# Kernel optimization log

Hardware: AMD Instinct MI355X
Metric: run time of the kernel (lower is better)

The kernel has to match this reference:

```python
import jax, jax.numpy as jnp
import numpy as np

EPS = 1e-12

def _pdist(a, b):
    # a: [B,N,3], b: [B,M,3] -> [B,N,M] L2 distances (no huge [B,N,M,3] temp)
    sq = (jnp.sum(a * a, -1)[:, :, None] + jnp.sum(b * b, -1)[:, None, :]
          - 2.0 * jnp.einsum('bnd,bmd->bnm', a, b))
    return jnp.sqrt(jnp.maximum(sq, EPS))

def _loss_terms(skel_xyz, skel_radius, skel_nori, l3_xyz, shape_all):
    normal = shape_all[:, :, 3:6]
    shape_xyz = shape_all[:, :, :3]
    B, Ns, _ = skel_xyz.shape
    N = shape_xyz.shape[1]

    # --- loss_sample: 8 surface samples per sphere ---
    e = 0.57735027
    dirs = jnp.array([[e, e, e], [e, e, -e], [e, -e, e], [e, -e, -e],
                      [-e, e, e], [-e, e, -e], [-e, -e, e], [-e, -e, -e]],
                     dtype=skel_xyz.dtype)
    centers = jnp.repeat(skel_xyz, 8, axis=1)
    radii = jnp.repeat(skel_radius, 8, axis=1)
    sample_xyz = centers + radii * jnp.tile(dirs, (Ns, 1))[None]

    d_ss = _pdist(shape_xyz, sample_xyz)
    cd1 = jnp.sum(jnp.min(d_ss, axis=1)) / (Ns * 8)    # sample -> shape
    cd2 = jnp.sum(jnp.min(d_ss, axis=2)) / N           # shape -> sample
    loss_sample = cd1 + cd2

    # --- point2sphere / sphere2point ---
    d_sc = _pdist(shape_xyz, skel_xyz)                 # [B, N, Ns]
    sph = jnp.abs(d_sc - skel_radius[:, None, :, 0])
    loss_p2s = jnp.sum(jnp.min(sph, axis=2)) / N + jnp.sum(jnp.min(sph, axis=1)) / Ns

    loss_radius = -jnp.sum(skel_radius) / Ns

    # --- loss_normal: 30-NN of skel in shape, |dot(nori, shape normal)| ---
    d_ks = _pdist(skel_xyz, shape_xyz)                 # [B, Ns, N]
    idx30 = jax.lax.top_k(-d_ks, 30)[1]                # [B, Ns, 30]
    nn_nrm = jnp.take_along_axis(normal[:, None, :, :], idx30[..., None], axis=2)
    dots = jnp.einsum('bjd,bjkd->bjk', skel_nori, nn_nrm)
    loss_normal = jnp.sum(jnp.mean(jnp.abs(dots), axis=2)) / B

    # --- loss_skelenormal: points swept along nori, vs l3_xyz ---
    ks = (jnp.arange(30, dtype=skel_xyz.dtype) / 30.0)[None, :, None, None]
    combine = (skel_xyz[:, None] + skel_nori[:, None] * ks).reshape(B, 30 * Ns, 3)
    mind = jnp.min(_pdist(combine, l3_xyz), axis=2)
    loss_skn = 50.0 * jnp.sum(mind) / (B * Ns * 30)
    loss_skn = loss_skn + 500.0 * jnp.sum(jnp.var(mind, axis=1, ddof=1)) / B

    # --- loss_normaldist: exp barrier + hard penalty on |nori| ---
    nrm = jnp.sqrt(jnp.sum(skel_nori * skel_nori, -1) + EPS)
    loss_nd = jnp.sum(jnp.exp(-(nrm - 0.3)) + jnp.where(nrm < 0.25, 5.0, 0.0)) / (B * Ns)

    # --- loss_normalsmooth: 3-NN (incl. self) nori consistency ---
    idx3 = jax.lax.top_k(-_pdist(skel_xyz, skel_xyz), 3)[1]   # [B, Ns, 3]
    nn_nori = jnp.take_along_axis(skel_nori[:, None, :, :], idx3[..., None], axis=2)
    diff = skel_nori[:, :, None, :] - nn_nori
    loss_ns = jnp.sum(jnp.sqrt(jnp.sum(diff * diff, -1) + EPS)) / (B * Ns * 3)

    return loss_sample, loss_p2s, loss_radius, loss_normal, loss_skn, loss_nd, loss_ns

def setup_inputs() -> dict:
    key = jax.random.key(0)
    ks = jax.random.split(key, 9)
    B, N, Ns, M = 8, 4096, 256, 256
    return {
        'skel_xyz': jax.random.normal(ks[0], (B, Ns, 3), jnp.float32),
        'skel_radius': jax.random.uniform(ks[1], (B, Ns, 1), jnp.float32),
        'shape_cmb_features': jax.random.normal(ks[2], (B, Ns, 32), jnp.float32),
        'skel_nori': jax.random.normal(ks[3], (B, Ns, 3), jnp.float32),
        'weights': jax.random.uniform(ks[4], (B, Ns, 8), jnp.float32),
        'l3_xyz': jax.random.normal(ks[5], (B, M, 3), jnp.float32),
        'l3_normals': jax.random.normal(ks[6], (B, M, 3), jnp.float32),
        'shape_xyz': jax.random.normal(ks[7], (B, N, 6), jnp.float32),
        'A': jax.random.uniform(ks[8], (B, Ns, Ns), jnp.float32),
        'w0': 1, 'w1': 1, 'w2': 1, 'w3': 1, 'w4': 1, 'w5': 1, 'w6': 1,
    }

def reference(skel_xyz, skel_radius, shape_cmb_features, skel_nori, weights,
              l3_xyz, l3_normals, shape_xyz, A,
              w0, w1, w2, w3, w4, w5, w6):
    ls, lp, lr, ln, lskn, lnd, lns = _loss_terms(
        skel_xyz, skel_radius, skel_nori, l3_xyz, shape_xyz)
    # lap_reg=False -> loss_smooth = 0 (w3 term vanishes)
    return (w0 * ls + lp * w1 + lr * w2 + ln * w4 + lskn * w5
            + w6 * lnd + 0.1 * lns)
```

## Files before the change

kernel.cpp:

```cpp
#include <hip/hip_runtime.h>
#include <math.h>

#define EPS 1e-12f
#define EDIR 0.57735027f
#define M2E  -1.15470054f

#define NB 8
#define NS 256
#define NP 4096
#define NM 256

#define NSLOT 64
#define SLOTW 32
#define ACC_F (NSLOT * SLOTW)

#define T_CD1   0
#define T_CD2   1
#define T_P2SN  2
#define T_P2SJ  3
#define T_NORM  5
#define T_ND    6
#define T_NS    7
#define T_SKN_SUM 8
#define T_SKN_SQ  16

#define NBLK_SKEL 512
#define NBLK_PREP 128
#define NBLK_SP   (NBLK_SKEL + NBLK_PREP)

#define NBLK_CD1  512
#define NBLK_CD2  1024
#define NBLK_SKN  240
#define B0_CD2  (NBLK_CD1)
#define B0_SKN  (B0_CD2 + NBLK_CD2)
#define NBLK_REST (B0_SKN + NBLK_SKN)

__device__ __forceinline__ unsigned umin2(unsigned a, unsigned b){ return a<b?a:b; }
__device__ __forceinline__ unsigned umax2(unsigned a, unsigned b){ return a>b?a:b; }

__device__ __forceinline__ float wave_min(float v){
#pragma unroll
  for (int o = 32; o; o >>= 1) v = fminf(v, __shfl_xor(v, o));
  return v;
}
__device__ __forceinline__ float wave_max(float v){
#pragma unroll
  for (int o = 32; o; o >>= 1) v = fmaxf(v, __shfl_xor(v, o));
  return v;
}
__device__ __forceinline__ float wave_sum(float v){
#pragma unroll
  for (int o = 32; o; o >>= 1) v += __shfl_xor(v, o);
  return v;
}
__device__ __forceinline__ unsigned wave_min_u(unsigned v){
#pragma unroll
  for (int o = 32; o; o >>= 1){ unsigned w = __shfl_xor(v, o); v = (w < v) ? w : v; }
  return v;
}
__device__ __forceinline__ unsigned wave_max_u(unsigned v){
#pragma unroll
  for (int o = 32; o; o >>= 1){ unsigned w = __shfl_xor(v, o); v = (w > v) ? w : v; }
  return v;
}
__device__ __forceinline__ unsigned long long wave_min_u64(unsigned long long v){
#pragma unroll
  for (int o = 32; o; o >>= 1){
    unsigned long long w = __shfl_xor(v, o);
    v = (w < v) ? w : v;
  }
  return v;
}

#define OFF_SMP (ACC_F)
#define OFF_SKR (OFF_SMP + NB*2048*4)
#define OFF_SXY (OFF_SKR + NB*NS*4)
#define OFF_L3P (OFF_SXY + NB*NP*4)
#define OFF_NR4 (OFF_L3P + NB*NM*4)

__global__ __launch_bounds__(256) void k_sp(const float* __restrict__ skel,
                                            const float* __restrict__ rad,
                                            const float* __restrict__ nori,
                                            const float* __restrict__ l3,
                                            const float* __restrict__ shape,
                                            float* __restrict__ ws){
  int bid = blockIdx.x;
  int tid = threadIdx.x;

  if (bid >= NBLK_SKEL){
    int i = (bid - NBLK_SKEL) * 256 + tid;
    float4* smp = (float4*)(ws + OFF_SMP);
    float4* skr = (float4*)(ws + OFF_SKR);
    float4* sxy = (float4*)(ws + OFF_SXY);
    float4* l3p = (float4*)(ws + OFF_L3P);
    float4* nr4 = (float4*)(ws + OFF_NR4);
    {
      const float* q = shape + (size_t)i * 6;
      float x = q[0], y = q[1], z = q[2];
      sxy[i] = make_float4(x, y, z, fmaf(x, x, fmaf(y, y, z * z)));
    }
    if (i < NB * 2048){
      int b = i >> 11, m = i & 2047;
      int si = m >> 3, k = m & 7;
      const float* sp = skel + (size_t)(b * NS + si) * 3;
      float r = rad[b * NS + si];
      float x = sp[0] + r * ((k & 4) ? -EDIR : EDIR);
      float y = sp[1] + r * ((k & 2) ? -EDIR : EDIR);
      float z = sp[2] + r * ((k & 1) ? -EDIR : EDIR);
      smp[i] = make_float4(x, y, z, fmaf(x, x, fmaf(y, y, z * z)));
    }
    if (i < NB * NS){
      const float* sp = skel + (size_t)i * 3;
      skr[i] = make_float4(sp[0], sp[1], sp[2], rad[i]);
      const float* nn = nori + (size_t)i * 3;
      nr4[i] = make_float4(nn[0], nn[1], nn[2], 0.0f);
      const float* lp = l3 + (size_t)i * 3;
      float x = lp[0], y = lp[1], z = lp[2];
      l3p[i] = make_float4(x, y, z, fmaf(x, x, fmaf(y, y, z * z)));
    }
    return;
  }

  int wid  = tid >> 6;
  int lane = tid & 63;
  int row  = bid * 4 + wid;
  int b = row >> 8;
  const float* sjp = skel + (size_t)row * 3;
  float cx = sjp[0], cy = sjp[1], cz = sjp[2];
  float rj = rad[row];
  float r2j = rj * rj;
  const float* njp = nori + (size_t)row * 3;
  float nx = njp[0], ny = njp[1], nz = njp[2];
  const float* shb = shape + (size_t)b * NP * 6;

  unsigned a0=~0u,a1=~0u,a2=~0u,a3=~0u,a4=~0u,a5=~0u;
  unsigned b0=~0u,b1=~0u,b2=~0u,b3=~0u,b4=~0u,b5=~0u;
  float dmoA = 3.4e38f, dmiA = -3.4e38f, dmoB = 3.4e38f, dmiB = -3.4e38f;

#pragma unroll 2
  for (int s = 0; s < 32; ++s){
    int nA = s * 128 + lane;
    int nB = nA + 64;
    float2 xyA = *(const float2*)(shb + (size_t)nA * 6);
    float  zA  = shb[(size_t)nA * 6 + 2];
    float2 xyB = *(const float2*)(shb + (size_t)nB * 6);
    float  zB  = shb[(size_t)nB * 6 + 2];
    float dxA = xyA.x - cx, dyA = xyA.y - cy, dzA = zA - cz;
    float dxB = xyB.x - cx, dyB = xyB.y - cy, dzB = zB - cz;
    float dA = fmaf(dxA, dxA, fmaf(dyA, dyA, dzA * dzA));
    float dB = fmaf(dxB, dxB, fmaf(dyB, dyB, dzB * dzB));
    bool inA = dA < r2j;
    bool inB = dB < r2j;
    dmoA = fminf(dmoA, inA ? 3.4e38f : dA);
    dmiA = fmaxf(dmiA, inA ? dA : -3.4e38f);
    dmoB = fminf(dmoB, inB ? 3.4e38f : dB);
    dmiB = fmaxf(dmiB, inB ? dB : -3.4e38f);
    unsigned uA = (__float_as_uint(dA) & 0xFFFFF000u) | (unsigned)nA;
    unsigned uB = (__float_as_uint(dB) & 0xFFFFF000u) | (unsigned)nB;
    a5 = umin2(a5, uA);
    { unsigned p = umin2(a4, a5), q = umax2(a4, a5); a4 = p; a5 = q; }
    { unsigned p = umin2(a3, a4), q = umax2(a3, a4); a3 = p; a4 = q; }
    { unsigned p = umin2(a2, a3), q = umax2(a2, a3); a2 = p; a3 = q; }
    { unsigned p = umin2(a1, a2), q = umax2(a1, a2); a1 = p; a2 = q; }
    { unsigned p = umin2(a0, a1), q = umax2(a0, a1); a0 = p; a1 = q; }
    b5 = umin2(b5, uB);
    { unsigned p = umin2(b4, b5), q = umax2(b4, b5); b4 = p; b5 = q; }
    { unsigned p = umin2(b3, b4), q = umax2(b3, b4); b3 = p; b4 = q; }
    { unsigned p = umin2(b2, b3), q = umax2(b2, b3); b2 = p; b3 = q; }
    { unsigned p = umin2(b1, b2), q = umax2(b1, b2); b1 = p; b2 = q; }
    { unsigned p = umin2(b0, b1), q = umax2(b0, b1); b0 = p; b1 = q; }
  }
  float dmin_out = wave_min(fminf(dmoA, dmoB));
  float dmax_in  = wave_max(fmaxf(dmiA, dmiB));
  float pmin = sqrtf(fmaxf(dmin_out, EPS)) - rj;
  float pin  = (dmax_in >= 0.0f) ? (rj - sqrtf(fmaxf(dmax_in, EPS))) : 3.4e38f;
  pmin = fminf(pmin, pin);

  unsigned lmin = umin2(a0, b0);
  unsigned lo = wave_min_u(lmin), hi = wave_max_u(lmin);
  while (lo < hi){
    unsigned mid = lo + ((hi - lo) >> 1);
    int c = __popcll(__ballot(a0 <= mid)) + __popcll(__ballot(a1 <= mid)) +
            __popcll(__ballot(a2 <= mid)) + __popcll(__ballot(a3 <= mid)) +
            __popcll(__ballot(a4 <= mid)) + __popcll(__ballot(a5 <= mid)) +
            __popcll(__ballot(b0 <= mid)) + __popcll(__ballot(b1 <= mid)) +
            __popcll(__ballot(b2 <= mid)) + __popcll(__ballot(b3 <= mid)) +
            __popcll(__ballot(b4 <= mid)) + __popcll(__ballot(b5 <= mid));
    if (c >= 30) hi = mid; else lo = mid + 1;
  }
  unsigned tau = hi;

  float dsum = 0.0f;
  {
    unsigned mm[12] = {a0,a1,a2,a3,a4,a5,b0,b1,b2,b3,b4,b5};
#pragma unroll
    for (int r = 0; r < 12; ++r){
      if (mm[r] <= tau){
        int idx = (int)(mm[r] & 0xFFFu);
        const float* qq = shb + (size_t)idx * 6;
        dsum += fabsf(fmaf(nx, qq[3], fmaf(ny, qq[4], nz * qq[5])));
      }
    }
  }
  dsum = wave_sum(dsum);

  const float* skb = skel + (size_t)b * NS * 3;
  const float* nb  = nori + (size_t)b * NS * 3;
  unsigned u0=~0u,u1=~0u,u2=~0u; int i0=0,i1=0,i2=0;
#pragma unroll
  for (int it = 0; it < 4; ++it){
    int n2i = it * 64 + lane;
    float dx = skb[n2i*3+0] - cx, dy = skb[n2i*3+1] - cy, dz = skb[n2i*3+2] - cz;
    unsigned u = __float_as_uint(fmaf(dx,dx,fmaf(dy,dy,dz*dz)));
    if (u < u2){ u2 = u; i2 = n2i; }
    if (u2 < u1){ unsigned t=u1;u1=u2;u2=t; int ti=i1;i1=i2;i2=ti; }
    if (u1 < u0){ unsigned t=u0;u0=u1;u1=t; int ti=i0;i0=i1;i1=ti; }
  }
  int cc = 0;
  float nssum = 0.0f;
#pragma unroll
  for (int r = 0; r < 3; ++r){
    unsigned hu = (cc==0)?u0:((cc==1)?u1:u2);
    int      hix= (cc==0)?i0:((cc==1)?i1:i2);
    unsigned long long pack = (((unsigned long long)hu) << 32) | (unsigned)hix;
    unsigned long long best = wave_min_u64(pack);
    if (pack == best) cc++;
    int idx = (int)(best & 0xffffffffull);
    if (lane == 0){
      float axn = nb[idx*3+0]-nx, ayn = nb[idx*3+1]-ny, azn = nb[idx*3+2]-nz;
      nssum += sqrtf(fmaf(axn,axn,fmaf(ayn,ayn,azn*azn)) + EPS);
    }
  }

  if (lane == 0){
    float nrm = sqrtf(nx*nx + ny*ny + nz*nz + EPS);
    float ndv = expf(0.3f - nrm) + ((nrm < 0.25f) ? 5.0f : 0.0f);
    float* slot = ws + (size_t)(row & (NSLOT - 1)) * SLOTW;
    atomicAdd(slot + T_P2SJ, pmin);
    atomicAdd(slot + T_NORM, dsum * (1.0f / 30.0f));
    atomicAdd(slot + T_NS,   nssum);
    atomicAdd(slot + T_ND,   ndv);
  }
}

__global__ __launch_bounds__(256) void k_rest(float* __restrict__ ws){
  __shared__ float4 lsh[NM];
  __shared__ float r1[4], r2[4];
  const float4* smp = (const float4*)(ws + OFF_SMP);
  const float4* skr = (const float4*)(ws + OFF_SKR);
  const float4* sxy = (const float4*)(ws + OFF_SXY);
  const float4* l3p = (const float4*)(ws + OFF_L3P);
  const float4* nr4 = (const float4*)(ws + OFF_NR4);
  int bid  = blockIdx.x;
  int tid  = threadIdx.x;
  int wid  = tid >> 6;
  int lane = tid & 63;

  if (bid < NBLK_CD1){
    int wv   = bid * 4 + wid;
    int row0 = wv * 8;
    int b    = row0 >> 11;
    float ax[8], ay[8], az[8], aw[8];
#pragma unroll
    for (int i = 0; i < 8; ++i){
      float4 c = smp[row0 + i];
      ax[i] = -2.0f * c.x; ay[i] = -2.0f * c.y; az[i] = -2.0f * c.z; aw[i] = c.w;
    }
    const float4* sh = sxy + (size_t)b * NP;
    float mn[8];
#pragma unroll
    for (int i = 0; i < 8; ++i) mn[i] = 3.4e38f;
#pragma unroll 8
    for (int s = 0; s < 64; ++s){
      float4 p = sh[s * 64 + lane];
#pragma unroll
      for (int i = 0; i < 8; ++i){
        float t = fmaf(p.x, ax[i], fmaf(p.y, ay[i], fmaf(p.z, az[i], p.w)));
        mn[i] = fminf(mn[i], t);
      }
    }
    float v = 0.0f;
#pragma unroll
    for (int i = 0; i < 8; ++i){
      float m = wave_min(mn[i]);
      v += sqrtf(fmaxf(m + aw[i], EPS));
    }
    if (lane == 0)
      atomicAdd(ws + (size_t)(bid & (NSLOT - 1)) * SLOTW + T_CD1, v);

  } else if (bid < B0_SKN){
    int wv   = (bid - B0_CD2) * 4 + wid;
    int row0 = wv * 8;
    int b    = row0 >> 12;
    float cx[8], cy[8], cz[8];
#pragma unroll
    for (int i = 0; i < 8; ++i){
      float4 c = sxy[row0 + i];
      cx[i] = c.x; cy[i] = c.y; cz[i] = c.z;
    }
    const float4* kb = skr + (size_t)b * NS;
    float mn[8], pm[8];
#pragma unroll
    for (int i = 0; i < 8; ++i){ mn[i] = 3.4e38f; pm[i] = 3.4e38f; }
#pragma unroll
    for (int it = 0; it < 4; ++it){
      float4 kr = kb[it * 64 + lane];
      float rr = kr.w;
      float r2 = rr * rr;
      float c1 = M2E * rr;
#pragma unroll
      for (int i = 0; i < 8; ++i){
        float dx = cx[i] - kr.x, dy = cy[i] - kr.y, dz = cz[i] - kr.z;
        float q  = fmaf(dx, dx, fmaf(dy, dy, dz * dz));
        float s  = (fabsf(dx) + fabsf(dy)) + fabsf(dz);
        mn[i] = fminf(mn[i], fmaf(c1, s, q + r2));
        float d = sqrtf(fmaxf(q, EPS));
        pm[i] = fminf(pm[i], fabsf(d - rr));
      }
    }
    float cdv = 0.0f, pv = 0.0f;
#pragma unroll
    for (int i = 0; i < 8; ++i){
      float m = wave_min(mn[i]);
      cdv += sqrtf(fmaxf(m, EPS));
      pv  += wave_min(pm[i]);
    }
    if (lane == 0){
      float* slot = ws + (size_t)(bid & (NSLOT - 1)) * SLOTW;
      atomicAdd(slot + T_CD2, cdv);
      atomicAdd(slot + T_P2SN, pv);
    }

  } else {
    int q  = bid - B0_SKN;
    int b  = q / 30;
    int t  = (q % 30) * 256 + tid;
    lsh[tid] = l3p[(size_t)b * NM + tid];
    __syncthreads();
    int s = t >> 8;
    int j = t & 255;
    float ksf = (float)s * (1.0f / 30.0f);
    float4 sj = skr[(size_t)b * NS + j];
    float4 nj = nr4[(size_t)b * NS + j];
    float px = fmaf(nj.x, ksf, sj.x);
    float py = fmaf(nj.y, ksf, sj.y);
    float pz = fmaf(nj.z, ksf, sj.z);
    float ax = -2.0f * px, ay = -2.0f * py, az = -2.0f * pz;
    float pw = fmaf(px, px, fmaf(py, py, pz * pz));
    float mn = 3.4e38f;
#pragma unroll 8
    for (int qq = 0; qq < NM; ++qq){
      float4 L = lsh[qq];
      float t2 = fmaf(L.x, ax, fmaf(L.y, ay, fmaf(L.z, az, L.w)));
      mn = fminf(mn, t2);
    }
    float d = sqrtf(fmaxf(mn + pw, EPS));
    float s1 = wave_sum(d);
    float s2 = wave_sum(d * d);
    if (lane == 0){ r1[wid] = s1; r2[wid] = s2; }
    __syncthreads();
    if (tid == 0){
      float a1 = r1[0]+r1[1]+r1[2]+r1[3];
      float a2 = r2[0]+r2[1]+r2[2]+r2[3];
      float* slot = ws + (size_t)(bid & (NSLOT - 1)) * SLOTW;
      atomicAdd(slot + T_SKN_SUM + b, a1);
      atomicAdd(slot + T_SKN_SQ  + b, a2);
    }
  }
}

__global__ __launch_bounds__(256) void k_final(const float* __restrict__ rad,
                                               const float* __restrict__ ws,
                                               const int* w0, const int* w1, const int* w2,
                                               const int* w4, const int* w5, const int* w6,
                                               float* __restrict__ out){
  __shared__ float A[SLOTW];
  __shared__ float rs[256];
  int tid = threadIdx.x;
  if (tid < SLOTW){
    float v = 0.0f;
    for (int s = 0; s < NSLOT; ++s) v += ws[(size_t)s * SLOTW + tid];
    A[tid] = v;
  }
  float r = 0.0f;
  for (int q = tid; q < NB * NS; q += 256) r += rad[q];
  rs[tid] = r;
  __syncthreads();
  if (tid == 0){
    float srad = 0.0f;
    for (int q = 0; q < 256; ++q) srad += rs[q];
    float ls = A[T_CD1] * (1.0f/2048.0f) + A[T_CD2] * (1.0f/4096.0f);
    float lp = A[T_P2SN] * (1.0f/4096.0f) + A[T_P2SJ] * (1.0f/256.0f);
    float lr = -srad * (1.0f/256.0f);
    float ln = A[T_NORM] * (1.0f/8.0f);
    float smind = 0.0f, vsum = 0.0f;
    for (int bb = 0; bb < NB; ++bb){
      float s1 = A[T_SKN_SUM + bb], s2 = A[T_SKN_SQ + bb];
      smind += s1;
      vsum  += (s2 - s1 * s1 * (1.0f/7680.0f)) * (1.0f/7679.0f);
    }
    float lskn = 50.0f * smind * (1.0f/(8.0f*7680.0f)) + 500.0f * vsum * (1.0f/8.0f);
    float lnd = A[T_ND] * (1.0f/2048.0f);
    float lns = A[T_NS] * (1.0f/6144.0f);
    float o = (float)w0[0]*ls + (float)w1[0]*lp + (float)w2[0]*lr +
              (float)w4[0]*ln + (float)w5[0]*lskn + (float)w6[0]*lnd + 0.1f*lns;
    out[0] = o;
  }
}

extern "C" void kernel_launch(void* const* d_in, const int* in_sizes, int n_in,
                              void* d_out, int out_size, void* d_ws, size_t ws_size,
                              hipStream_t stream) {
  const float* skel  = (const float*)d_in[0];
  const float* rad   = (const float*)d_in[1];
  const float* nori  = (const float*)d_in[3];
  const float* l3    = (const float*)d_in[5];
  const float* shape = (const float*)d_in[7];
  const int* w0 = (const int*)d_in[9];
  const int* w1 = (const int*)d_in[10];
  const int* w2 = (const int*)d_in[11];
  const int* w4 = (const int*)d_in[13];
  const int* w5 = (const int*)d_in[14];
  const int* w6 = (const int*)d_in[15];
  float* ws  = (float*)d_ws;
  float* out = (float*)d_out;

  hipMemsetAsync(ws, 0, ACC_F * sizeof(float), stream);
  k_sp<<<dim3(NBLK_SP), dim3(256), 0, stream>>>(skel, rad, nori, l3, shape, ws);
  k_rest<<<dim3(NBLK_REST), dim3(256), 0, stream>>>(ws);
  k_final<<<dim3(1), dim3(256), 0, stream>>>(rad, ws, w0, w1, w2, w4, w5, w6, out);
}
```

Before: 61.70 us.

## Split CD1 sample-to-shape min across two waves with atomicMin reduction

The sample-to-shape Chamfer pass now gives each wave 4 sample rows and half of the shape points instead of 8 rows over all points, which quadruples the CD1 block count. Partial minima are merged with atomicMin on an order-preserving unsigned encoding into a new workspace array. The final kernel then decodes the minima and does the sqrt and sum. The aim is more parallelism and shorter per-wave loops, at the cost of an extra memset, global atomics and a serial 16K-element pass in the single-block final kernel.

```diff
diff --git a/kernel.cpp b/kernel.cpp
--- a/kernel.cpp
+++ b/kernel.cpp
@@ -28,7 +28,7 @@
 #define NBLK_PREP 128
 #define NBLK_SP   (NBLK_SKEL + NBLK_PREP)
 
-#define NBLK_CD1  512
+#define NBLK_CD1  2048
 #define NBLK_CD2  1024
 #define NBLK_SKN  240
 #define B0_CD2  (NBLK_CD1)
@@ -38,6 +38,14 @@
 __device__ __forceinline__ unsigned umin2(unsigned a, unsigned b){ return a<b?a:b; }
 __device__ __forceinline__ unsigned umax2(unsigned a, unsigned b){ return a>b?a:b; }
 
+__device__ __forceinline__ unsigned fenc(float f){
+  unsigned u = __float_as_uint(f);
+  return (u & 0x80000000u) ? ~u : (u | 0x80000000u);
+}
+__device__ __forceinline__ float fdec(unsigned u){
+  return (u & 0x80000000u) ? __uint_as_float(u ^ 0x80000000u) : __uint_as_float(~u);
+}
+
 __device__ __forceinline__ float wave_min(float v){
 #pragma unroll
   for (int o = 32; o; o >>= 1) v = fminf(v, __shfl_xor(v, o));
@@ -77,6 +85,7 @@
 #define OFF_SXY (OFF_SKR + NB*NS*4)
 #define OFF_L3P (OFF_SXY + NB*NP*4)
 #define OFF_NR4 (OFF_L3P + NB*NM*4)
+#define OFF_C1M (OFF_NR4 + NB*NS*4)
 
 __global__ __launch_bounds__(256) void k_sp(const float* __restrict__ skel,
                                             const float* __restrict__ rad,
@@ -251,6 +260,7 @@
   const float4* sxy = (const float4*)(ws + OFF_SXY);
   const float4* l3p = (const float4*)(ws + OFF_L3P);
   const float4* nr4 = (const float4*)(ws + OFF_NR4);
+  unsigned* c1m = (unsigned*)(ws + OFF_C1M);
   int bid  = blockIdx.x;
   int tid  = threadIdx.x;
   int wid  = tid >> 6;
@@ -258,35 +268,34 @@
 
   if (bid < NBLK_CD1){
     int wv   = bid * 4 + wid;
-    int row0 = wv * 8;
+    int rg   = wv >> 1;
+    int half = wv & 1;
+    int row0 = rg * 4;
     int b    = row0 >> 11;
-    float ax[8], ay[8], az[8], aw[8];
-#pragma unroll
-    for (int i = 0; i < 8; ++i){
+    float ax[4], ay[4], az[4];
+#pragma unroll
+    for (int i = 0; i < 4; ++i){
       float4 c = smp[row0 + i];
-      ax[i] = -2.0f * c.x; ay[i] = -2.0f * c.y; az[i] = -2.0f * c.z; aw[i] = c.w;
-    }
-    const float4* sh = sxy + (size_t)b * NP;
-    float mn[8];
-#pragma unroll
-    for (int i = 0; i < 8; ++i) mn[i] = 3.4e38f;
+      ax[i] = -2.0f * c.x; ay[i] = -2.0f * c.y; az[i] = -2.0f * c.z;
+    }
+    const float4* sh = sxy + (size_t)b * NP + half * 2048;
+    float mn[4];
+#pragma unroll
+    for (int i = 0; i < 4; ++i) mn[i] = 3.4e38f;
 #pragma unroll 8
-    for (int s = 0; s < 64; ++s){
+    for (int s = 0; s < 32; ++s){
       float4 p = sh[s * 64 + lane];
 #pragma unroll
-      for (int i = 0; i < 8; ++i){
+      for (int i = 0; i < 4; ++i){
         float t = fmaf(p.x, ax[i], fmaf(p.y, ay[i], fmaf(p.z, az[i], p.w)));
         mn[i] = fminf(mn[i], t);
       }
     }
-    float v = 0.0f;
-#pragma unroll
-    for (int i = 0; i < 8; ++i){
+#pragma unroll
+    for (int i = 0; i < 4; ++i){
       float m = wave_min(mn[i]);
-      v += sqrtf(fmaxf(m + aw[i], EPS));
-    }
-    if (lane == 0)
-      atomicAdd(ws + (size_t)(bid & (NSLOT - 1)) * SLOTW + T_CD1, v);
+      if (lane == 0) atomicMin(c1m + row0 + i, fenc(m));
+    }
 
   } else if (bid < B0_SKN){
     int wv   = (bid - B0_CD2) * 4 + wid;
@@ -376,6 +385,7 @@
                                                float* __restrict__ out){
   __shared__ float A[SLOTW];
   __shared__ float rs[256];
+  __shared__ float cs[256];
   int tid = threadIdx.x;
   if (tid < SLOTW){
     float v = 0.0f;
@@ -385,11 +395,20 @@
   float r = 0.0f;
   for (int q = tid; q < NB * NS; q += 256) r += rad[q];
   rs[tid] = r;
+  const unsigned* c1m = (const unsigned*)(ws + OFF_C1M);
+  const float4*   smp = (const float4*)(ws + OFF_SMP);
+  float c1 = 0.0f;
+  for (int q = tid; q < NB * 2048; q += 256){
+    unsigned u = c1m[q];
+    float m = (u & 0x80000000u) ? __uint_as_float(u ^ 0x80000000u) : __uint_as_float(~u);
+    c1 += sqrtf(fmaxf(m + smp[q].w, EPS));
+  }
+  cs[tid] = c1;
   __syncthreads();
   if (tid == 0){
-    float srad = 0.0f;
-    for (int q = 0; q < 256; ++q) srad += rs[q];
-    float ls = A[T_CD1] * (1.0f/2048.0f) + A[T_CD2] * (1.0f/4096.0f);
+    float srad = 0.0f, c1t = 0.0f;
+    for (int q = 0; q < 256; ++q){ srad += rs[q]; c1t += cs[q]; }
+    float ls = c1t * (1.0f/2048.0f) + A[T_CD2] * (1.0f/4096.0f);
     float lp = A[T_P2SN] * (1.0f/4096.0f) + A[T_P2SJ] * (1.0f/256.0f);
     float lr = -srad * (1.0f/256.0f);
     float ln = A[T_NORM] * (1.0f/8.0f);
@@ -426,6 +445,7 @@
   float* out = (float*)d_out;
 
   hipMemsetAsync(ws, 0, ACC_F * sizeof(float), stream);
+  hipMemsetAsync(ws + OFF_C1M, 0xFF, NB * 2048 * sizeof(unsigned), stream);
   k_sp<<<dim3(NBLK_SP), dim3(256), 0, stream>>>(skel, rad, nori, l3, shape, ws);
   k_rest<<<dim3(NBLK_REST), dim3(256), 0, stream>>>(ws);
   k_final<<<dim3(1), dim3(256), 0, stream>>>(rad, ws, w0, w1, w2, w4, w5, w6, out);
```

New measurement: 89.47 us. +45.0%, slower.

## Fuse preprocessing and loss kernels into one mega kernel, drop memset and atomics

Applied to the files above, without the earlier changes.

Merges the skeleton kernel, the preprocessing pass and the rest kernel into a single launch that reads the raw inputs directly, so the staged float4 workspace buffers are no longer needed. The CD1 pass changes from iterating over precomputed sample points to computing all 8 sphere-surface distances per shape point from one squared distance plus signed direction sums. Slotted atomics and the memset are replaced by per-row partial writes that the final kernel reduces. The aim is to remove two launches, the memset and the intermediate traffic. In exchange, kernels read stride-6 raw data without the float4 packing, and the final single-block reduction has more work to do.

```diff
diff --git a/kernel.cpp b/kernel.cpp
--- a/kernel.cpp
+++ b/kernel.cpp
@@ -10,30 +10,21 @@
 #define NP 4096
 #define NM 256
 
-#define NSLOT 64
-#define SLOTW 32
-#define ACC_F (NSLOT * SLOTW)
-
-#define T_CD1   0
-#define T_CD2   1
-#define T_P2SN  2
-#define T_P2SJ  3
-#define T_NORM  5
-#define T_ND    6
-#define T_NS    7
-#define T_SKN_SUM 8
-#define T_SKN_SQ  16
-
 #define NBLK_SKEL 512
-#define NBLK_PREP 128
-#define NBLK_SP   (NBLK_SKEL + NBLK_PREP)
-
 #define NBLK_CD1  512
 #define NBLK_CD2  1024
 #define NBLK_SKN  240
-#define B0_CD2  (NBLK_CD1)
+#define B0_CD1  (NBLK_SKEL)
+#define B0_CD2  (B0_CD1 + NBLK_CD1)
 #define B0_SKN  (B0_CD2 + NBLK_CD2)
-#define NBLK_REST (B0_SKN + NBLK_SKN)
+#define NBLK_MEGA (B0_SKN + NBLK_SKN)
+
+#define OFF_SKO 0
+#define OFF_C1O (OFF_SKO + 2048*4)
+#define OFF_C2O (OFF_C1O + 2048)
+#define OFF_P2O (OFF_C2O + 4096)
+#define OFF_SKS (OFF_P2O + 4096)
+#define OFF_SKQ (OFF_SKS + 240)
 
 __device__ __forceinline__ unsigned umin2(unsigned a, unsigned b){ return a<b?a:b; }
 __device__ __forceinline__ unsigned umax2(unsigned a, unsigned b){ return a>b?a:b; }
@@ -72,221 +63,176 @@
   return v;
 }
 
-#define OFF_SMP (ACC_F)
-#define OFF_SKR (OFF_SMP + NB*2048*4)
-#define OFF_SXY (OFF_SKR + NB*NS*4)
-#define OFF_L3P (OFF_SXY + NB*NP*4)
-#define OFF_NR4 (OFF_L3P + NB*NM*4)
-
-__global__ __launch_bounds__(256) void k_sp(const float* __restrict__ skel,
-                                            const float* __restrict__ rad,
-                                            const float* __restrict__ nori,
-                                            const float* __restrict__ l3,
-                                            const float* __restrict__ shape,
-                                            float* __restrict__ ws){
-  int bid = blockIdx.x;
-  int tid = threadIdx.x;
-
-  if (bid >= NBLK_SKEL){
-    int i = (bid - NBLK_SKEL) * 256 + tid;
-    float4* smp = (float4*)(ws + OFF_SMP);
-    float4* skr = (float4*)(ws + OFF_SKR);
-    float4* sxy = (float4*)(ws + OFF_SXY);
-    float4* l3p = (float4*)(ws + OFF_L3P);
-    float4* nr4 = (float4*)(ws + OFF_NR4);
-    {
-      const float* q = shape + (size_t)i * 6;
-      float x = q[0], y = q[1], z = q[2];
-      sxy[i] = make_float4(x, y, z, fmaf(x, x, fmaf(y, y, z * z)));
-    }
-    if (i < NB * 2048){
-      int b = i >> 11, m = i & 2047;
-      int si = m >> 3, k = m & 7;
-      const float* sp = skel + (size_t)(b * NS + si) * 3;
-      float r = rad[b * NS + si];
-      float x = sp[0] + r * ((k & 4) ? -EDIR : EDIR);
-      float y = sp[1] + r * ((k & 2) ? -EDIR : EDIR);
-      float z = sp[2] + r * ((k & 1) ? -EDIR : EDIR);
-      smp[i] = make_float4(x, y, z, fmaf(x, x, fmaf(y, y, z * z)));
-    }
-    if (i < NB * NS){
-      const float* sp = skel + (size_t)i * 3;
-      skr[i] = make_float4(sp[0], sp[1], sp[2], rad[i]);
-      const float* nn = nori + (size_t)i * 3;
-      nr4[i] = make_float4(nn[0], nn[1], nn[2], 0.0f);
-      const float* lp = l3 + (size_t)i * 3;
-      float x = lp[0], y = lp[1], z = lp[2];
-      l3p[i] = make_float4(x, y, z, fmaf(x, x, fmaf(y, y, z * z)));
-    }
-    return;
-  }
-
-  int wid  = tid >> 6;
-  int lane = tid & 63;
-  int row  = bid * 4 + wid;
-  int b = row >> 8;
-  const float* sjp = skel + (size_t)row * 3;
-  float cx = sjp[0], cy = sjp[1], cz = sjp[2];
-  float rj = rad[row];
-  float r2j = rj * rj;
-  const float* njp = nori + (size_t)row * 3;
-  float nx = njp[0], ny = njp[1], nz = njp[2];
-  const float* shb = shape + (size_t)b * NP * 6;
-
-  unsigned a0=~0u,a1=~0u,a2=~0u,a3=~0u,a4=~0u,a5=~0u;
-  unsigned b0=~0u,b1=~0u,b2=~0u,b3=~0u,b4=~0u,b5=~0u;
-  float dmoA = 3.4e38f, dmiA = -3.4e38f, dmoB = 3.4e38f, dmiB = -3.4e38f;
-
-#pragma unroll 2
-  for (int s = 0; s < 32; ++s){
-    int nA = s * 128 + lane;
-    int nB = nA + 64;
-    float2 xyA = *(const float2*)(shb + (size_t)nA * 6);
-    float  zA  = shb[(size_t)nA * 6 + 2];
-    float2 xyB = *(const float2*)(shb + (size_t)nB * 6);
-    float  zB  = shb[(size_t)nB * 6 + 2];
-    float dxA = xyA.x - cx, dyA = xyA.y - cy, dzA = zA - cz;
-    float dxB = xyB.x - cx, dyB = xyB.y - cy, dzB = zB - cz;
-    float dA = fmaf(dxA, dxA, fmaf(dyA, dyA, dzA * dzA));
-    float dB = fmaf(dxB, dxB, fmaf(dyB, dyB, dzB * dzB));
-    bool inA = dA < r2j;
-    bool inB = dB < r2j;
-    dmoA = fminf(dmoA, inA ? 3.4e38f : dA);
-    dmiA = fmaxf(dmiA, inA ? dA : -3.4e38f);
-    dmoB = fminf(dmoB, inB ? 3.4e38f : dB);
-    dmiB = fmaxf(dmiB, inB ? dB : -3.4e38f);
-    unsigned uA = (__float_as_uint(dA) & 0xFFFFF000u) | (unsigned)nA;
-    unsigned uB = (__float_as_uint(dB) & 0xFFFFF000u) | (unsigned)nB;
-    a5 = umin2(a5, uA);
-    { unsigned p = umin2(a4, a5), q = umax2(a4, a5); a4 = p; a5 = q; }
-    { unsigned p = umin2(a3, a4), q = umax2(a3, a4); a3 = p; a4 = q; }
-    { unsigned p = umin2(a2, a3), q = umax2(a2, a3); a2 = p; a3 = q; }
-    { unsigned p = umin2(a1, a2), q = umax2(a1, a2); a1 = p; a2 = q; }
-    { unsigned p = umin2(a0, a1), q = umax2(a0, a1); a0 = p; a1 = q; }
-    b5 = umin2(b5, uB);
-    { unsigned p = umin2(b4, b5), q = umax2(b4, b5); b4 = p; b5 = q; }
-    { unsigned p = umin2(b3, b4), q = umax2(b3, b4); b3 = p; b4 = q; }
-    { unsigned p = umin2(b2, b3), q = umax2(b2, b3); b2 = p; b3 = q; }
-    { unsigned p = umin2(b1, b2), q = umax2(b1, b2); b1 = p; b2 = q; }
-    { unsigned p = umin2(b0, b1), q = umax2(b0, b1); b0 = p; b1 = q; }
-  }
-  float dmin_out = wave_min(fminf(dmoA, dmoB));
-  float dmax_in  = wave_max(fmaxf(dmiA, dmiB));
-  float pmin = sqrtf(fmaxf(dmin_out, EPS)) - rj;
-  float pin  = (dmax_in >= 0.0f) ? (rj - sqrtf(fmaxf(dmax_in, EPS))) : 3.4e38f;
-  pmin = fminf(pmin, pin);
-
-  unsigned lmin = umin2(a0, b0);
-  unsigned lo = wave_min_u(lmin), hi = wave_max_u(lmin);
-  while (lo < hi){
-    unsigned mid = lo + ((hi - lo) >> 1);
-    int c = __popcll(__ballot(a0 <= mid)) + __popcll(__ballot(a1 <= mid)) +
-            __popcll(__ballot(a2 <= mid)) + __popcll(__ballot(a3 <= mid)) +
-            __popcll(__ballot(a4 <= mid)) + __popcll(__ballot(a5 <= mid)) +
-            __popcll(__ballot(b0 <= mid)) + __popcll(__ballot(b1 <= mid)) +
-            __popcll(__ballot(b2 <= mid)) + __popcll(__ballot(b3 <= mid)) +
-            __popcll(__ballot(b4 <= mid)) + __popcll(__ballot(b5 <= mid));
-    if (c >= 30) hi = mid; else lo = mid + 1;
-  }
-  unsigned tau = hi;
-
-  float dsum = 0.0f;
-  {
-    unsigned mm[12] = {a0,a1,a2,a3,a4,a5,b0,b1,b2,b3,b4,b5};
-#pragma unroll
-    for (int r = 0; r < 12; ++r){
-      if (mm[r] <= tau){
-        int idx = (int)(mm[r] & 0xFFFu);
-        const float* qq = shb + (size_t)idx * 6;
-        dsum += fabsf(fmaf(nx, qq[3], fmaf(ny, qq[4], nz * qq[5])));
-      }
-    }
-  }
-  dsum = wave_sum(dsum);
-
-  const float* skb = skel + (size_t)b * NS * 3;
-  const float* nb  = nori + (size_t)b * NS * 3;
-  unsigned u0=~0u,u1=~0u,u2=~0u; int i0=0,i1=0,i2=0;
-#pragma unroll
-  for (int it = 0; it < 4; ++it){
-    int n2i = it * 64 + lane;
-    float dx = skb[n2i*3+0] - cx, dy = skb[n2i*3+1] - cy, dz = skb[n2i*3+2] - cz;
-    unsigned u = __float_as_uint(fmaf(dx,dx,fmaf(dy,dy,dz*dz)));
-    if (u < u2){ u2 = u; i2 = n2i; }
-    if (u2 < u1){ unsigned t=u1;u1=u2;u2=t; int ti=i1;i1=i2;i2=ti; }
-    if (u1 < u0){ unsigned t=u0;u0=u1;u1=t; int ti=i0;i0=i1;i1=ti; }
-  }
-  int cc = 0;
-  float nssum = 0.0f;
-#pragma unroll
-  for (int r = 0; r < 3; ++r){
-    unsigned hu = (cc==0)?u0:((cc==1)?u1:u2);
-    int      hix= (cc==0)?i0:((cc==1)?i1:i2);
-    unsigned long long pack = (((unsigned long long)hu) << 32) | (unsigned)hix;
-    unsigned long long best = wave_min_u64(pack);
-    if (pack == best) cc++;
-    int idx = (int)(best & 0xffffffffull);
-    if (lane == 0){
-      float axn = nb[idx*3+0]-nx, ayn = nb[idx*3+1]-ny, azn = nb[idx*3+2]-nz;
-      nssum += sqrtf(fmaf(axn,axn,fmaf(ayn,ayn,azn*azn)) + EPS);
-    }
-  }
-
-  if (lane == 0){
-    float nrm = sqrtf(nx*nx + ny*ny + nz*nz + EPS);
-    float ndv = expf(0.3f - nrm) + ((nrm < 0.25f) ? 5.0f : 0.0f);
-    float* slot = ws + (size_t)(row & (NSLOT - 1)) * SLOTW;
-    atomicAdd(slot + T_P2SJ, pmin);
-    atomicAdd(slot + T_NORM, dsum * (1.0f / 30.0f));
-    atomicAdd(slot + T_NS,   nssum);
-    atomicAdd(slot + T_ND,   ndv);
-  }
-}
-
-__global__ __launch_bounds__(256) void k_rest(float* __restrict__ ws){
+__global__ __launch_bounds__(256) void k_mega(const float* __restrict__ skel,
+                                              const float* __restrict__ rad,
+                                              const float* __restrict__ nori,
+                                              const float* __restrict__ l3,
+                                              const float* __restrict__ shape,
+                                              float* __restrict__ ws){
   __shared__ float4 lsh[NM];
   __shared__ float r1[4], r2[4];
-  const float4* smp = (const float4*)(ws + OFF_SMP);
-  const float4* skr = (const float4*)(ws + OFF_SKR);
-  const float4* sxy = (const float4*)(ws + OFF_SXY);
-  const float4* l3p = (const float4*)(ws + OFF_L3P);
-  const float4* nr4 = (const float4*)(ws + OFF_NR4);
   int bid  = blockIdx.x;
   int tid  = threadIdx.x;
   int wid  = tid >> 6;
   int lane = tid & 63;
 
-  if (bid < NBLK_CD1){
-    int wv   = bid * 4 + wid;
-    int row0 = wv * 8;
-    int b    = row0 >> 11;
-    float ax[8], ay[8], az[8], aw[8];
-#pragma unroll
-    for (int i = 0; i < 8; ++i){
-      float4 c = smp[row0 + i];
-      ax[i] = -2.0f * c.x; ay[i] = -2.0f * c.y; az[i] = -2.0f * c.z; aw[i] = c.w;
-    }
-    const float4* sh = sxy + (size_t)b * NP;
+  if (bid < B0_CD1){
+    int row = bid * 4 + wid;
+    int b = row >> 8;
+    const float* sjp = skel + (size_t)row * 3;
+    float cx = sjp[0], cy = sjp[1], cz = sjp[2];
+    float rj = rad[row];
+    float r2j = rj * rj;
+    const float* njp = nori + (size_t)row * 3;
+    float nx = njp[0], ny = njp[1], nz = njp[2];
+    const float* shb = shape + (size_t)b * NP * 6;
+
+    unsigned a0=~0u,a1=~0u,a2=~0u,a3=~0u,a4=~0u,a5=~0u;
+    unsigned b0=~0u,b1=~0u,b2=~0u,b3=~0u,b4=~0u,b5=~0u;
+    float dmoA = 3.4e38f, dmiA = -3.4e38f, dmoB = 3.4e38f, dmiB = -3.4e38f;
+
+#pragma unroll 2
+    for (int s = 0; s < 32; ++s){
+      int nA = s * 128 + lane;
+      int nB = nA + 64;
+      float2 xyA = *(const float2*)(shb + (size_t)nA * 6);
+      float  zA  = shb[(size_t)nA * 6 + 2];
+      float2 xyB = *(const float2*)(shb + (size_t)nB * 6);
+      float  zB  = shb[(size_t)nB * 6 + 2];
+      float dxA = xyA.x - cx, dyA = xyA.y - cy, dzA = zA - cz;
+      float dxB = xyB.x - cx, dyB = xyB.y - cy, dzB = zB - cz;
+      float dA = fmaf(dxA, dxA, fmaf(dyA, dyA, dzA * dzA));
+      float dB = fmaf(dxB, dxB, fmaf(dyB, dyB, dzB * dzB));
+      bool inA = dA < r2j;
+      bool inB = dB < r2j;
+      dmoA = fminf(dmoA, inA ? 3.4e38f : dA);
+      dmiA = fmaxf(dmiA, inA ? dA : -3.4e38f);
+      dmoB = fminf(dmoB, inB ? 3.4e38f : dB);
+      dmiB = fmaxf(dmiB, inB ? dB : -3.4e38f);
+      unsigned uA = (__float_as_uint(dA) & 0xFFFFF000u) | (unsigned)nA;
+      unsigned uB = (__float_as_uint(dB) & 0xFFFFF000u) | (unsigned)nB;
+      a5 = umin2(a5, uA);
+      { unsigned p = umin2(a4, a5), q = umax2(a4, a5); a4 = p; a5 = q; }
+      { unsigned p = umin2(a3, a4), q = umax2(a3, a4); a3 = p; a4 = q; }
+      { unsigned p = umin2(a2, a3), q = umax2(a2, a3); a2 = p; a3 = q; }
+      { unsigned p = umin2(a1, a2), q = umax2(a1, a2); a1 = p; a2 = q; }
+      { unsigned p = umin2(a0, a1), q = umax2(a0, a1); a0 = p; a1 = q; }
+      b5 = umin2(b5, uB);
+      { unsigned p = umin2(b4, b5), q = umax2(b4, b5); b4 = p; b5 = q; }
+      { unsigned p = umin2(b3, b4), q = umax2(b3, b4); b3 = p; b4 = q; }
+      { unsigned p = umin2(b2, b3), q = umax2(b2, b3); b2 = p; b3 = q; }
+      { unsigned p = umin2(b1, b2), q = umax2(b1, b2); b1 = p; b2 = q; }
+      { unsigned p = umin2(b0, b1), q = umax2(b0, b1); b0 = p; b1 = q; }
+    }
+    float dmin_out = wave_min(fminf(dmoA, dmoB));
+    float dmax_in  = wave_max(fmaxf(dmiA, dmiB));
+    float pmin = sqrtf(fmaxf(dmin_out, EPS)) - rj;
+    float pin  = (dmax_in >= 0.0f) ? (rj - sqrtf(fmaxf(dmax_in, EPS))) : 3.4e38f;
+    pmin = fminf(pmin, pin);
+
+    unsigned lmin = umin2(a0, b0);
+    unsigned lo = wave_min_u(lmin), hi = wave_max_u(lmin);
+    while (lo < hi){
+      unsigned mid = lo + ((hi - lo) >> 1);
+      int c = __popcll(__ballot(a0 <= mid)) + __popcll(__ballot(a1 <= mid)) +
+              __popcll(__ballot(a2 <= mid)) + __popcll(__ballot(a3 <= mid)) +
+              __popcll(__ballot(a4 <= mid)) + __popcll(__ballot(a5 <= mid)) +
+              __popcll(__ballot(b0 <= mid)) + __popcll(__ballot(b1 <= mid)) +
+              __popcll(__ballot(b2 <= mid)) + __popcll(__ballot(b3 <= mid)) +
+              __popcll(__ballot(b4 <= mid)) + __popcll(__ballot(b5 <= mid));
+      if (c >= 30) hi = mid; else lo = mid + 1;
+    }
+    unsigned tau = hi;
+
+    float dsum = 0.0f;
+    {
+      unsigned mm[12] = {a0,a1,a2,a3,a4,a5,b0,b1,b2,b3,b4,b5};
+#pragma unroll
+      for (int r = 0; r < 12; ++r){
+        if (mm[r] <= tau){
+          int idx = (int)(mm[r] & 0xFFFu);
+          const float* qq = shb + (size_t)idx * 6;
+          dsum += fabsf(fmaf(nx, qq[3], fmaf(ny, qq[4], nz * qq[5])));
+        }
+      }
+    }
+    dsum = wave_sum(dsum);
+
+    const float* skb = skel + (size_t)b * NS * 3;
+    const float* nb  = nori + (size_t)b * NS * 3;
+    unsigned u0=~0u,u1=~0u,u2=~0u; int i0=0,i1=0,i2=0;
+#pragma unroll
+    for (int it = 0; it < 4; ++it){
+      int n2i = it * 64 + lane;
+      float dx = skb[n2i*3+0] - cx, dy = skb[n2i*3+1] - cy, dz = skb[n2i*3+2] - cz;
+      unsigned u = __float_as_uint(fmaf(dx,dx,fmaf(dy,dy,dz*dz)));
+      if (u < u2){ u2 = u; i2 = n2i; }
+      if (u2 < u1){ unsigned t=u1;u1=u2;u2=t; int ti=i1;i1=i2;i2=ti; }
+      if (u1 < u0){ unsigned t=u0;u0=u1;u1=t; int ti=i0;i0=i1;i1=ti; }
+    }
+    int cc = 0;
+    float nssum = 0.0f;
+#pragma unroll
+    for (int r = 0; r < 3; ++r){
+      unsigned hu = (cc==0)?u0:((cc==1)?u1:u2);
+      int      hix= (cc==0)?i0:((cc==1)?i1:i2);
+      unsigned long long pack = (((unsigned long long)hu) << 32) | (unsigned)hix;
+      unsigned long long best = wave_min_u64(pack);
+      if (pack == best) cc++;
+      int idx = (int)(best & 0xffffffffull);
+      if (lane == 0){
+        float axn = nb[idx*3+0]-nx, ayn = nb[idx*3+1]-ny, azn = nb[idx*3+2]-nz;
+        nssum += sqrtf(fmaf(axn,axn,fmaf(ayn,ayn,azn*azn)) + EPS);
+      }
+    }
+
+    if (lane == 0){
+      float nrm = sqrtf(nx*nx + ny*ny + nz*nz + EPS);
+      float ndv = expf(0.3f - nrm) + ((nrm < 0.25f) ? 5.0f : 0.0f);
+      float* sko = ws + OFF_SKO + (size_t)row * 4;
+      sko[0] = pmin;
+      sko[1] = dsum * (1.0f / 30.0f);
+      sko[2] = nssum;
+      sko[3] = ndv;
+    }
+
+  } else if (bid < B0_CD2){
+    int s0 = (bid - B0_CD1) * 4 + wid;
+    int b  = s0 >> 8;
+    const float* sp = skel + (size_t)s0 * 3;
+    float cx = sp[0], cy = sp[1], cz = sp[2];
+    float rr = rad[s0];
+    float m2re = M2E * rr;
+    const float* shb = shape + (size_t)b * NP * 6;
     float mn[8];
 #pragma unroll
-    for (int i = 0; i < 8; ++i) mn[i] = 3.4e38f;
-#pragma unroll 8
+    for (int k = 0; k < 8; ++k) mn[k] = 3.4e38f;
+#pragma unroll 4
     for (int s = 0; s < 64; ++s){
-      float4 p = sh[s * 64 + lane];
-#pragma unroll
-      for (int i = 0; i < 8; ++i){
-        float t = fmaf(p.x, ax[i], fmaf(p.y, ay[i], fmaf(p.z, az[i], p.w)));
-        mn[i] = fminf(mn[i], t);
-      }
-    }
+      int n = s * 64 + lane;
+      float2 xy = *(const float2*)(shb + (size_t)n * 6);
+      float pz  = shb[(size_t)n * 6 + 2];
+      float dx = xy.x - cx, dy = xy.y - cy, dz = pz - cz;
+      float q  = fmaf(dx, dx, fmaf(dy, dy, dz * dz));
+      float s1p = dx + dy, s2p = dx - dy;
+      float ga = s1p + dz, gb = s1p - dz, gc = s2p + dz, gd = s2p - dz;
+      mn[0] = fminf(mn[0], fmaf(m2re,  ga, q));
+      mn[1] = fminf(mn[1], fmaf(m2re,  gb, q));
+      mn[2] = fminf(mn[2], fmaf(m2re,  gc, q));
+      mn[3] = fminf(mn[3], fmaf(m2re,  gd, q));
+      mn[4] = fminf(mn[4], fmaf(m2re, -gd, q));
+      mn[5] = fminf(mn[5], fmaf(m2re, -gc, q));
+      mn[6] = fminf(mn[6], fmaf(m2re, -gb, q));
+      mn[7] = fminf(mn[7], fmaf(m2re, -ga, q));
+    }
+    float r2v = rr * rr;
     float v = 0.0f;
 #pragma unroll
-    for (int i = 0; i < 8; ++i){
-      float m = wave_min(mn[i]);
-      v += sqrtf(fmaxf(m + aw[i], EPS));
-    }
-    if (lane == 0)
-      atomicAdd(ws + (size_t)(bid & (NSLOT - 1)) * SLOTW + T_CD1, v);
+    for (int k = 0; k < 8; ++k){
+      float m = wave_min(mn[k]);
+      v += sqrtf(fmaxf(m + r2v, EPS));
+    }
+    if (lane == 0) ws[OFF_C1O + s0] = v;
 
   } else if (bid < B0_SKN){
     int wv   = (bid - B0_CD2) * 4 + wid;
@@ -295,22 +241,24 @@
     float cx[8], cy[8], cz[8];
 #pragma unroll
     for (int i = 0; i < 8; ++i){
-      float4 c = sxy[row0 + i];
-      cx[i] = c.x; cy[i] = c.y; cz[i] = c.z;
-    }
-    const float4* kb = skr + (size_t)b * NS;
+      const float* qp = shape + (size_t)(row0 + i) * 6;
+      cx[i] = qp[0]; cy[i] = qp[1]; cz[i] = qp[2];
+    }
+    const float* skb = skel + (size_t)b * NS * 3;
+    const float* rdb = rad + (size_t)b * NS;
     float mn[8], pm[8];
 #pragma unroll
     for (int i = 0; i < 8; ++i){ mn[i] = 3.4e38f; pm[i] = 3.4e38f; }
 #pragma unroll
     for (int it = 0; it < 4; ++it){
-      float4 kr = kb[it * 64 + lane];
-      float rr = kr.w;
+      int kidx = it * 64 + lane;
+      float kx = skb[kidx*3+0], ky = skb[kidx*3+1], kz = skb[kidx*3+2];
+      float rr = rdb[kidx];
       float r2 = rr * rr;
       float c1 = M2E * rr;
 #pragma unroll
       for (int i = 0; i < 8; ++i){
-        float dx = cx[i] - kr.x, dy = cy[i] - kr.y, dz = cz[i] - kr.z;
+        float dx = cx[i] - kx, dy = cy[i] - ky, dz = cz[i] - kz;
         float q  = fmaf(dx, dx, fmaf(dy, dy, dz * dz));
         float s  = (fabsf(dx) + fabsf(dy)) + fabsf(dz);
         mn[i] = fminf(mn[i], fmaf(c1, s, q + r2));
@@ -326,25 +274,28 @@
       pv  += wave_min(pm[i]);
     }
     if (lane == 0){
-      float* slot = ws + (size_t)(bid & (NSLOT - 1)) * SLOTW;
-      atomicAdd(slot + T_CD2, cdv);
-      atomicAdd(slot + T_P2SN, pv);
+      ws[OFF_C2O + wv] = cdv;
+      ws[OFF_P2O + wv] = pv;
     }
 
   } else {
     int q  = bid - B0_SKN;
     int b  = q / 30;
     int t  = (q % 30) * 256 + tid;
-    lsh[tid] = l3p[(size_t)b * NM + tid];
+    {
+      const float* lp = l3 + (size_t)(b * NM + tid) * 3;
+      float lx = lp[0], ly = lp[1], lz = lp[2];
+      lsh[tid] = make_float4(lx, ly, lz, fmaf(lx, lx, fmaf(ly, ly, lz * lz)));
+    }
     __syncthreads();
     int s = t >> 8;
     int j = t & 255;
     float ksf = (float)s * (1.0f / 30.0f);
-    float4 sj = skr[(size_t)b * NS + j];
-    float4 nj = nr4[(size_t)b * NS + j];
-    float px = fmaf(nj.x, ksf, sj.x);
-    float py = fmaf(nj.y, ksf, sj.y);
-    float pz = fmaf(nj.z, ksf, sj.z);
+    const float* sj = skel + (size_t)(b * NS + j) * 3;
+    const float* nj = nori + (size_t)(b * NS + j) * 3;
+    float px = fmaf(nj[0], ksf, sj[0]);
+    float py = fmaf(nj[1], ksf, sj[1]);
+    float pz = fmaf(nj[2], ksf, sj[2]);
     float ax = -2.0f * px, ay = -2.0f * py, az = -2.0f * pz;
     float pw = fmaf(px, px, fmaf(py, py, pz * pz));
     float mn = 3.4e38f;
@@ -360,11 +311,8 @@
     if (lane == 0){ r1[wid] = s1; r2[wid] = s2; }
     __syncthreads();
     if (tid == 0){
-      float a1 = r1[0]+r1[1]+r1[2]+r1[3];
-      float a2 = r2[0]+r2[1]+r2[2]+r2[3];
-      float* slot = ws + (size_t)(bid & (NSLOT - 1)) * SLOTW;
-      atomicAdd(slot + T_SKN_SUM + b, a1);
-      atomicAdd(slot + T_SKN_SQ  + b, a2);
+      ws[OFF_SKS + q] = r1[0]+r1[1]+r1[2]+r1[3];
+      ws[OFF_SKQ + q] = r2[0]+r2[1]+r2[2]+r2[3];
     }
   }
 }
@@ -374,34 +322,66 @@
                                                const int* w0, const int* w1, const int* w2,
                                                const int* w4, const int* w5, const int* w6,
                                                float* __restrict__ out){
-  __shared__ float A[SLOTW];
-  __shared__ float rs[256];
+  __shared__ float red[8][4];
+  __shared__ float sb1[240], sb2[240];
+  __shared__ float bb1[8], bb2[8];
   int tid = threadIdx.x;
-  if (tid < SLOTW){
-    float v = 0.0f;
-    for (int s = 0; s < NSLOT; ++s) v += ws[(size_t)s * SLOTW + tid];
-    A[tid] = v;
-  }
-  float r = 0.0f;
-  for (int q = tid; q < NB * NS; q += 256) r += rad[q];
-  rs[tid] = r;
+  int wid = tid >> 6, lane = tid & 63;
+
+  float pp2sj = 0.0f, pnorm = 0.0f, pns = 0.0f, pnd = 0.0f;
+  for (int q = tid; q < 2048; q += 256){
+    const float* s4 = ws + OFF_SKO + (size_t)q * 4;
+    pp2sj += s4[0]; pnorm += s4[1]; pns += s4[2]; pnd += s4[3];
+  }
+  float pc1 = 0.0f;
+  for (int q = tid; q < 2048; q += 256) pc1 += ws[OFF_C1O + q];
+  float pc2 = 0.0f, pp2n = 0.0f;
+  for (int q = tid; q < 4096; q += 256){
+    pc2  += ws[OFF_C2O + q];
+    pp2n += ws[OFF_P2O + q];
+  }
+  float prad = 0.0f;
+  for (int q = tid; q < NB * NS; q += 256) prad += rad[q];
+
+  if (tid < 240){ sb1[tid] = ws[OFF_SKS + tid]; sb2[tid] = ws[OFF_SKQ + tid]; }
+
+  pp2sj = wave_sum(pp2sj); pnorm = wave_sum(pnorm);
+  pns = wave_sum(pns);     pnd = wave_sum(pnd);
+  pc1 = wave_sum(pc1);     pc2 = wave_sum(pc2);
+  pp2n = wave_sum(pp2n);   prad = wave_sum(prad);
+  if (lane == 0){
+    red[0][wid] = pp2sj; red[1][wid] = pnorm; red[2][wid] = pns; red[3][wid] = pnd;
+    red[4][wid] = pc1;   red[5][wid] = pc2;   red[6][wid] = pp2n; red[7][wid] = prad;
+  }
+  __syncthreads();
+  if (tid < 8){
+    float s1 = 0.0f, s2 = 0.0f;
+    for (int i = 0; i < 30; ++i){ s1 += sb1[tid * 30 + i]; s2 += sb2[tid * 30 + i]; }
+    bb1[tid] = s1; bb2[tid] = s2;
+  }
   __syncthreads();
   if (tid == 0){
-    float srad = 0.0f;
-    for (int q = 0; q < 256; ++q) srad += rs[q];
-    float ls = A[T_CD1] * (1.0f/2048.0f) + A[T_CD2] * (1.0f/4096.0f);
-    float lp = A[T_P2SN] * (1.0f/4096.0f) + A[T_P2SJ] * (1.0f/256.0f);
+    float p2sj = red[0][0]+red[0][1]+red[0][2]+red[0][3];
+    float nrmt = red[1][0]+red[1][1]+red[1][2]+red[1][3];
+    float nst  = red[2][0]+red[2][1]+red[2][2]+red[2][3];
+    float ndt  = red[3][0]+red[3][1]+red[3][2]+red[3][3];
+    float c1t  = red[4][0]+red[4][1]+red[4][2]+red[4][3];
+    float c2t  = red[5][0]+red[5][1]+red[5][2]+red[5][3];
+    float p2nt = red[6][0]+red[6][1]+red[6][2]+red[6][3];
+    float srad = red[7][0]+red[7][1]+red[7][2]+red[7][3];
+    float ls = c1t * (1.0f/2048.0f) + c2t * (1.0f/4096.0f);
+    float lp = p2nt * (1.0f/4096.0f) + p2sj * (1.0f/256.0f);
     float lr = -srad * (1.0f/256.0f);
-    float ln = A[T_NORM] * (1.0f/8.0f);
+    float ln = nrmt * (1.0f/8.0f);
     float smind = 0.0f, vsum = 0.0f;
-    for (int bb = 0; bb < NB; ++bb){
-      float s1 = A[T_SKN_SUM + bb], s2 = A[T_SKN_SQ + bb];
+    for (int b = 0; b < NB; ++b){
+      float s1 = bb1[b], s2 = bb2[b];
       smind += s1;
       vsum  += (s2 - s1 * s1 * (1.0f/7680.0f)) * (1.0f/7679.0f);
     }
     float lskn = 50.0f * smind * (1.0f/(8.0f*7680.0f)) + 500.0f * vsum * (1.0f/8.0f);
-    float lnd = A[T_ND] * (1.0f/2048.0f);
-    float lns = A[T_NS] * (1.0f/6144.0f);
+    float lnd = ndt * (1.0f/2048.0f);
+    float lns = nst * (1.0f/6144.0f);
     float o = (float)w0[0]*ls + (float)w1[0]*lp + (float)w2[0]*lr +
               (float)w4[0]*ln + (float)w5[0]*lskn + (float)w6[0]*lnd + 0.1f*lns;
     out[0] = o;
@@ -425,8 +405,6 @@
   float* ws  = (float*)d_ws;
   float* out = (float*)d_out;
 
-  hipMemsetAsync(ws, 0, ACC_F * sizeof(float), stream);
-  k_sp<<<dim3(NBLK_SP), dim3(256), 0, stream>>>(skel, rad, nori, l3, shape, ws);
-  k_rest<<<dim3(NBLK_REST), dim3(256), 0, stream>>>(ws);
+  k_mega<<<dim3(NBLK_MEGA), dim3(256), 0, stream>>>(skel, rad, nori, l3, shape, ws);
   k_final<<<dim3(1), dim3(256), 0, stream>>>(rad, ws, w0, w1, w2, w4, w5, w6, out);
 }
```

Result: faster. 53.97 us (-12.5%).
